# Performance work log

Measured on AMD Instinct MI355X. Metric: run time of the kernel, lower is better.

The kernel has to match this reference:

```python
import jax, jax.numpy as jnp
import numpy as np

C = 64
CR = C // 16  # reduction=16 -> query/key channels
B, H, W = 2, 80, 80


def setup_inputs() -> dict:
    key = jax.random.key(0)
    ks = jax.random.split(key, 13)
    s = 0.05
    return {
        "a": jax.random.normal(ks[0], (B, C, H, W), jnp.float32),
        "b": jax.random.normal(ks[1], (B, C, H, W), jnp.float32),
        "c": jax.random.normal(ks[2], (B, C, H, W), jnp.float32),
        # attentionAB (queries from a, keys from b)
        "wq_ab": jax.random.normal(ks[3], (CR, C), jnp.float32) * s,
        "bq_ab": jax.random.normal(ks[4], (CR,), jnp.float32) * s,
        "wk_ab": jax.random.normal(ks[5], (CR, C), jnp.float32) * s,
        "bk_ab": jax.random.normal(ks[6], (CR,), jnp.float32) * s,
        # attentionBC (queries from c, keys from b)
        "wq_bc": jax.random.normal(ks[7], (CR, C), jnp.float32) * s,
        "bq_bc": jax.random.normal(ks[8], (CR,), jnp.float32) * s,
        "wk_bc": jax.random.normal(ks[9], (CR, C), jnp.float32) * s,
        "bk_bc": jax.random.normal(ks[10], (CR,), jnp.float32) * s,
        # outer value conv on b
        "wv": jax.random.normal(ks[11], (C, C), jnp.float32) * s,
        "bv": jax.random.normal(ks[12], (C,), jnp.float32) * s,
    }


def _proj(x_flat, w, bias):
    # conv1x1 on flattened [B, C, N] -> [B, D, N]
    return jnp.einsum("dc,bcn->bdn", w, x_flat) + bias[None, :, None]


def _attention(x1_flat, x2_flat, wq, bq, wk, bk):
    q = _proj(x1_flat, wq, bq)  # [B, CR, N1]
    k = _proj(x2_flat, wk, bk)  # [B, CR, N2]
    scores = jnp.einsum("bdn,bdm->bnm", q, k)  # [B, N1, N2]
    return jax.nn.softmax(scores, axis=-1)


def reference(a, b, c, wq_ab, bq_ab, wk_ab, bk_ab, wq_bc, bq_bc, wk_bc, bk_bc, wv, bv):
    bsz, ch, h, w = b.shape
    n = h * w
    af = a.reshape(bsz, ch, n)
    bf = b.reshape(bsz, ch, n)
    cf = c.reshape(bsz, ch, n)

    attn_ba = _attention(af, bf, wq_ab, bq_ab, wk_ab, bk_ab)  # [B, Na, Nb]
    attn_bc = _attention(cf, bf, wq_bc, bq_bc, wk_bc, bk_bc)  # [B, Nc, Nb]

    values_b = _proj(bf, wv, bv)  # [B, C, Nb]

    # bmm(values_b, attn^T): contract over key positions m (of b)
    enh_ba = jnp.einsum("bcm,bnm->bcn", values_b, attn_ba)
    enh_bc = jnp.einsum("bcm,bnm->bcn", values_b, attn_bc)
    enhanced = (enh_ba + enh_bc) * 0.5
    return enhanced.reshape(bsz, ch, h, w)
```

## Files before the change

### kernel.cpp

```cpp
#include <hip/hip_runtime.h>
#include <hip/hip_bf16.h>

#define NPIX 6400
#define LOG2E 1.44269504088896340736f

typedef _Float16 half_t;
typedef _Float16 half4 __attribute__((ext_vector_type(4)));
typedef float float4x __attribute__((ext_vector_type(4)));


__global__ __launch_bounds__(256) void qk_proj_kernel(
    const float* __restrict__ a, const float* __restrict__ b, const float* __restrict__ c,
    const float* __restrict__ wq_ab, const float* __restrict__ bq_ab,
    const float* __restrict__ wk_ab, const float* __restrict__ bk_ab,
    const float* __restrict__ wq_bc, const float* __restrict__ bq_bc,
    const float* __restrict__ wk_bc, const float* __restrict__ bk_bc,
    half_t* __restrict__ qp, half_t* __restrict__ kp)
{
    int tid = blockIdx.x * 256 + threadIdx.x;
    int bz = tid / NPIX, n = tid % NPIX;
    const float* A = a + bz * 64 * NPIX + n;
    const float* B = b + bz * 64 * NPIX + n;
    const float* C = c + bz * 64 * NPIX + n;
    float qab[4] = {0,0,0,0}, kab[4] = {0,0,0,0}, qbc[4] = {0,0,0,0}, kbc[4] = {0,0,0,0};
    for (int ch = 0; ch < 64; ++ch) {
        float av = A[ch * NPIX], bv = B[ch * NPIX], cv = C[ch * NPIX];
#pragma unroll
        for (int d = 0; d < 4; ++d) {
            qab[d] += wq_ab[d * 64 + ch] * av;
            kab[d] += wk_ab[d * 64 + ch] * bv;
            qbc[d] += wq_bc[d * 64 + ch] * cv;
            kbc[d] += wk_bc[d * 64 + ch] * bv;
        }
    }
    half_t* q0 = qp + ((bz * 2 + 0) * NPIX + n) * 4;
    half_t* q1 = qp + ((bz * 2 + 1) * NPIX + n) * 4;
    half_t* k0 = kp + ((bz * 2 + 0) * NPIX + n) * 4;
    half_t* k1 = kp + ((bz * 2 + 1) * NPIX + n) * 4;
#pragma unroll
    for (int d = 0; d < 4; ++d) {
        q0[d] = (half_t)((qab[d] + bq_ab[d]) * LOG2E);
        q1[d] = (half_t)((qbc[d] + bq_bc[d]) * LOG2E);
        k0[d] = (half_t)(kab[d] + bk_ab[d]);
        k1[d] = (half_t)(kbc[d] + bk_bc[d]);
    }
}

__global__ __launch_bounds__(256) void v_proj_kernel(
    const float* __restrict__ b, const float* __restrict__ wv,
    const float* __restrict__ bvb, half_t* __restrict__ vp)
{
    int tid = blockIdx.x * 256 + threadIdx.x;
    int bz = tid / (64 * NPIX);
    int c  = (tid / NPIX) & 63;
    int n  = tid % NPIX;
    const float* B = b + bz * 64 * NPIX + n;
    float acc = bvb[c];
    for (int ch = 0; ch < 64; ++ch) acc += wv[c * 64 + ch] * B[ch * NPIX];
    vp[tid] = (half_t)acc;
}


__global__ __launch_bounds__(256) void attn_kernel(
    const half_t* __restrict__ qp, const half_t* __restrict__ kp,
    const half_t* __restrict__ vp, float* __restrict__ num, float* __restrict__ lsum)
{
    int idx = blockIdx.x;
    int qc = idx % 100;
    int br = (idx / 100) & 1;
    int bz = (idx / 200) & 1;
    int kh = idx / 400;
    int tid = threadIdx.x;
    int lane = tid & 63, w = tid >> 6;
    int g = lane >> 4, qi = lane & 15;
    int qbase = qc * 64 + w * 16;

    const half_t* Q = qp + ((bz * 2 + br) * NPIX + qbase) * 4;
    const half_t* K = kp + (bz * 2 + br) * NPIX * 4;
    const half_t* V = vp + bz * 64 * NPIX;

    half4 qf = {(half_t)0, (half_t)0, (half_t)0, (half_t)0};
    if (lane < 16) qf = *(const half4*)(Q + lane * 4);

    float4x accs[4] = {{0,0,0,0},{0,0,0,0},{0,0,0,0},{0,0,0,0}};
    float lrun = 0.f;

    __shared__ char lds[64 * 144];

    for (int chn = 0; chn < 50; ++chn) {
        int m0 = (kh * 50 + chn) * 64;
        __syncthreads();
#pragma unroll
        for (int si = 0; si < 2; ++si) {
            int s = tid + si * 256;
            int cc = s >> 3, so = s & 7;
            float4x seg = *(const float4x*)(V + cc * NPIX + m0 + so * 8);
            *(float4x*)(lds + cc * 144 + so * 16) = seg;
        }
        __syncthreads();
#pragma unroll
        for (int t = 0; t < 4; ++t) {
            int mt = m0 + t * 16;
            half4 kf = {(half_t)0, (half_t)0, (half_t)0, (half_t)0};
            if (lane < 16) kf = *(const half4*)(K + (mt + lane) * 4);
            float4x zero = {0.f, 0.f, 0.f, 0.f};
            float4x sc = __builtin_amdgcn_mfma_f32_16x16x16f16(kf, qf, zero, 0, 0, 0);
            float p0 = exp2f(sc[0]), p1 = exp2f(sc[1]), p2 = exp2f(sc[2]), p3 = exp2f(sc[3]);
            lrun += (p0 + p1) + (p2 + p3);
            half4 pf = {(half_t)p0, (half_t)p1, (half_t)p2, (half_t)p3};
            const char* lrow = lds + t * 32 + g * 8;
#pragma unroll
            for (int cb = 0; cb < 4; ++cb) {
                half4 vf = *(const half4*)(lrow + (cb * 16 + qi) * 144);
                accs[cb] = __builtin_amdgcn_mfma_f32_16x16x16f16(vf, pf, accs[cb], 0, 0, 0);
            }
        }
    }

    lrun += __shfl_xor(lrun, 16, 64);
    lrun += __shfl_xor(lrun, 32, 64);
    int q = qbase + qi;
    if (g == 0) atomicAdd(&lsum[(bz * 2 + br) * NPIX + q], lrun);

    float* numb = num + (bz * 2 + br) * 64 * NPIX;
#pragma unroll
    for (int cb = 0; cb < 4; ++cb)
#pragma unroll
        for (int r = 0; r < 4; ++r)
            atomicAdd(&numb[(cb * 16 + 4 * g + r) * NPIX + q], accs[cb][r]);
}

__global__ __launch_bounds__(256) void norm_kernel(
    const float* __restrict__ num, const float* __restrict__ lsum, float* __restrict__ out)
{
    int tid = blockIdx.x * 256 + threadIdx.x;
    int bz = tid / (64 * NPIX);
    int c  = (tid / NPIX) & 63;
    int n  = tid % NPIX;
    float lA = lsum[(bz * 2 + 0) * NPIX + n];
    float lC = lsum[(bz * 2 + 1) * NPIX + n];
    float vA = num[((bz * 2 + 0) * 64 + c) * NPIX + n];
    float vC = num[((bz * 2 + 1) * 64 + c) * NPIX + n];
    out[tid] = 0.5f * (vA / lA + vC / lC);
}

extern "C" void kernel_launch(void* const* d_in, const int* in_sizes, int n_in,
                              void* d_out, int out_size, void* d_ws, size_t ws_size,
                              hipStream_t stream) {
    (void)in_sizes; (void)n_in; (void)out_size; (void)ws_size;
    const float* a     = (const float*)d_in[0];
    const float* b     = (const float*)d_in[1];
    const float* c     = (const float*)d_in[2];
    const float* wq_ab = (const float*)d_in[3];
    const float* bq_ab = (const float*)d_in[4];
    const float* wk_ab = (const float*)d_in[5];
    const float* bk_ab = (const float*)d_in[6];
    const float* wq_bc = (const float*)d_in[7];
    const float* bq_bc = (const float*)d_in[8];
    const float* wk_bc = (const float*)d_in[9];
    const float* bk_bc = (const float*)d_in[10];
    const float* wv    = (const float*)d_in[11];
    const float* bv    = (const float*)d_in[12];
    float* out = (float*)d_out;

    half_t* qp = (half_t*)d_ws;
    half_t* kp = qp + 2 * 2 * NPIX * 4;
    half_t* vp = kp + 2 * 2 * NPIX * 4;
    float* num  = (float*)(vp + 2 * 64 * NPIX);
    float* lsum = num + 2 * 2 * 64 * NPIX;

    hipMemsetAsync(num, 0, (size_t)(2 * 2 * 64 * NPIX + 2 * 2 * NPIX) * sizeof(float), stream);

    qk_proj_kernel<<<50, 256, 0, stream>>>(a, b, c, wq_ab, bq_ab, wk_ab, bk_ab,
                                           wq_bc, bq_bc, wk_bc, bk_bc, qp, kp);
    v_proj_kernel<<<3200, 256, 0, stream>>>(b, wv, bv, vp);
    attn_kernel<<<800, 256, 0, stream>>>(qp, kp, vp, num, lsum);
    norm_kernel<<<3200, 256, 0, stream>>>(num, lsum, out);
}
```

Baseline: 220.3 us.

## Restructure attention with double-buffered LDS, two query tiles per wave, and vectorized projections

The attention kernel now handles 32 queries per wave across two MFMA tiles. This reuses each LDS V fragment and K fragment twice, and it splits keys into 4 chunks instead of 2. V tiles and K fragments are prefetched into registers and double-buffered in LDS so that one barrier per chunk overlaps loads with compute, and block indices are swizzled. The QK projection spreads the 4 output dims across threads for more parallelism, and the V projection and normalization are vectorized to float4 using a fast reciprocal. This raises register pressure and doubles the atomic contention on the numerator.

Result: faster. 213.4 us (-3.1%).

```diff
diff --git a/kernel.cpp b/kernel.cpp
--- a/kernel.cpp
+++ b/kernel.cpp
@@ -3,6 +3,10 @@
 
 #define NPIX 6400
 #define LOG2E 1.44269504088896340736f
+#define KH 4
+#define KEYS 1600
+#define NCH 25
+#define QF 2
 
 typedef _Float16 half_t;
 typedef _Float16 half4 __attribute__((ext_vector_type(4)));
@@ -18,32 +22,25 @@
     half_t* __restrict__ qp, half_t* __restrict__ kp)
 {
     int tid = blockIdx.x * 256 + threadIdx.x;
-    int bz = tid / NPIX, n = tid % NPIX;
+    int d = tid & 3;
+    int n = (tid >> 2) % NPIX;
+    int bz = (tid >> 2) / NPIX;
     const float* A = a + bz * 64 * NPIX + n;
     const float* B = b + bz * 64 * NPIX + n;
     const float* C = c + bz * 64 * NPIX + n;
-    float qab[4] = {0,0,0,0}, kab[4] = {0,0,0,0}, qbc[4] = {0,0,0,0}, kbc[4] = {0,0,0,0};
+    float qab = 0.f, kab = 0.f, qbc = 0.f, kbc = 0.f;
+#pragma unroll 4
     for (int ch = 0; ch < 64; ++ch) {
         float av = A[ch * NPIX], bv = B[ch * NPIX], cv = C[ch * NPIX];
-#pragma unroll
-        for (int d = 0; d < 4; ++d) {
-            qab[d] += wq_ab[d * 64 + ch] * av;
-            kab[d] += wk_ab[d * 64 + ch] * bv;
-            qbc[d] += wq_bc[d * 64 + ch] * cv;
-            kbc[d] += wk_bc[d * 64 + ch] * bv;
-        }
-    }
-    half_t* q0 = qp + ((bz * 2 + 0) * NPIX + n) * 4;
-    half_t* q1 = qp + ((bz * 2 + 1) * NPIX + n) * 4;
-    half_t* k0 = kp + ((bz * 2 + 0) * NPIX + n) * 4;
-    half_t* k1 = kp + ((bz * 2 + 1) * NPIX + n) * 4;
-#pragma unroll
-    for (int d = 0; d < 4; ++d) {
-        q0[d] = (half_t)((qab[d] + bq_ab[d]) * LOG2E);
-        q1[d] = (half_t)((qbc[d] + bq_bc[d]) * LOG2E);
-        k0[d] = (half_t)(kab[d] + bk_ab[d]);
-        k1[d] = (half_t)(kbc[d] + bk_bc[d]);
-    }
+        qab += wq_ab[d * 64 + ch] * av;
+        kab += wk_ab[d * 64 + ch] * bv;
+        qbc += wq_bc[d * 64 + ch] * cv;
+        kbc += wk_bc[d * 64 + ch] * bv;
+    }
+    qp[((bz * 2 + 0) * NPIX + n) * 4 + d] = (half_t)((qab + bq_ab[d]) * LOG2E);
+    qp[((bz * 2 + 1) * NPIX + n) * 4 + d] = (half_t)((qbc + bq_bc[d]) * LOG2E);
+    kp[((bz * 2 + 0) * NPIX + n) * 4 + d] = (half_t)(kab + bk_ab[d]);
+    kp[((bz * 2 + 1) * NPIX + n) * 4 + d] = (half_t)(kbc + bk_bc[d]);
 }
 
 __global__ __launch_bounds__(256) void v_proj_kernel(
@@ -51,13 +48,19 @@
     const float* __restrict__ bvb, half_t* __restrict__ vp)
 {
     int tid = blockIdx.x * 256 + threadIdx.x;
-    int bz = tid / (64 * NPIX);
-    int c  = (tid / NPIX) & 63;
-    int n  = tid % NPIX;
-    const float* B = b + bz * 64 * NPIX + n;
-    float acc = bvb[c];
-    for (int ch = 0; ch < 64; ++ch) acc += wv[c * 64 + ch] * B[ch * NPIX];
-    vp[tid] = (half_t)acc;
+    int n4 = tid % 1600;
+    int c  = (tid / 1600) & 63;
+    int bz = tid / (1600 * 64);
+    const float* B = b + bz * 64 * NPIX + n4 * 4;
+    float bias = bvb[c];
+    float4x acc = {bias, bias, bias, bias};
+    for (int ch = 0; ch < 64; ++ch) {
+        float4x bv = *(const float4x*)(B + ch * NPIX);
+        float wcc = wv[c * 64 + ch];
+        acc += wcc * bv;
+    }
+    half4 hv = {(half_t)acc[0], (half_t)acc[1], (half_t)acc[2], (half_t)acc[3]};
+    *(half4*)(vp + (bz * 64 + c) * NPIX + n4 * 4) = hv;
 }
 
 
@@ -65,83 +68,121 @@
     const half_t* __restrict__ qp, const half_t* __restrict__ kp,
     const half_t* __restrict__ vp, float* __restrict__ num, float* __restrict__ lsum)
 {
-    int idx = blockIdx.x;
-    int qc = idx % 100;
-    int br = (idx / 100) & 1;
-    int bz = (idx / 200) & 1;
-    int kh = idx / 400;
+    int bid = blockIdx.x;
+    int swz = (bid & 7) * 100 + (bid >> 3);
+    int qc = swz % 50;
+    int br = (swz / 50) & 1;
+    int bz = (swz / 100) & 1;
+    int kh = swz / 200;
+
     int tid = threadIdx.x;
     int lane = tid & 63, w = tid >> 6;
     int g = lane >> 4, qi = lane & 15;
-    int qbase = qc * 64 + w * 16;
+    int qbase = qc * 128 + w * 32;
 
     const half_t* Q = qp + ((bz * 2 + br) * NPIX + qbase) * 4;
-    const half_t* K = kp + (bz * 2 + br) * NPIX * 4;
-    const half_t* V = vp + bz * 64 * NPIX;
-
-    half4 qf = {(half_t)0, (half_t)0, (half_t)0, (half_t)0};
-    if (lane < 16) qf = *(const half4*)(Q + lane * 4);
-
-    float4x accs[4] = {{0,0,0,0},{0,0,0,0},{0,0,0,0},{0,0,0,0}};
-    float lrun = 0.f;
-
-    __shared__ char lds[64 * 144];
-
-    for (int chn = 0; chn < 50; ++chn) {
-        int m0 = (kh * 50 + chn) * 64;
-        __syncthreads();
-#pragma unroll
-        for (int si = 0; si < 2; ++si) {
-            int s = tid + si * 256;
-            int cc = s >> 3, so = s & 7;
-            float4x seg = *(const float4x*)(V + cc * NPIX + m0 + so * 8);
-            *(float4x*)(lds + cc * 144 + so * 16) = seg;
+    const half_t* K = kp + ((bz * 2 + br) * NPIX + kh * KEYS) * 4;
+    const half_t* V = vp + bz * 64 * NPIX + kh * KEYS;
+
+    half4 hz = {(half_t)0, (half_t)0, (half_t)0, (half_t)0};
+    half4 qf[QF];
+#pragma unroll
+    for (int i = 0; i < QF; ++i)
+        qf[i] = (lane < 16) ? *(const half4*)(Q + (i * 16 + lane) * 4) : hz;
+
+    float4x accs[QF][4] = {{{0,0,0,0},{0,0,0,0},{0,0,0,0},{0,0,0,0}},
+                           {{0,0,0,0},{0,0,0,0},{0,0,0,0},{0,0,0,0}}};
+    float lrun[QF] = {0.f, 0.f};
+
+    __shared__ char lds[2][64 * 144];
+    int cc0 = tid >> 3, so0 = tid & 7;
+    int cc1 = cc0 + 32;
+
+    float4x ga = *(const float4x*)(V + cc0 * NPIX + so0 * 8);
+    float4x gb = *(const float4x*)(V + cc1 * NPIX + so0 * 8);
+    half4 kc[4];
+#pragma unroll
+    for (int t = 0; t < 4; ++t)
+        kc[t] = (lane < 16) ? *(const half4*)(K + (t * 16 + lane) * 4) : hz;
+    *(float4x*)(lds[0] + cc0 * 144 + so0 * 16) = ga;
+    *(float4x*)(lds[0] + cc1 * 144 + so0 * 16) = gb;
+    __syncthreads();
+
+    int cur = 0;
+    for (int chn = 0; chn < NCH; ++chn) {
+        bool more = (chn + 1 < NCH);
+        float4x gna, gnb;
+        half4 kn[4];
+        if (more) {
+            int m0n = (chn + 1) * 64;
+            gna = *(const float4x*)(V + cc0 * NPIX + m0n + so0 * 8);
+            gnb = *(const float4x*)(V + cc1 * NPIX + m0n + so0 * 8);
+#pragma unroll
+            for (int t = 0; t < 4; ++t)
+                kn[t] = (lane < 16) ? *(const half4*)(K + (m0n + t * 16 + lane) * 4) : hz;
+        }
+        const char* lb = lds[cur];
+#pragma unroll
+        for (int t = 0; t < 4; ++t) {
+            half4 vf[4];
+#pragma unroll
+            for (int cb = 0; cb < 4; ++cb)
+                vf[cb] = *(const half4*)(lb + (cb * 16 + qi) * 144 + t * 32 + g * 8);
+#pragma unroll
+            for (int i = 0; i < QF; ++i) {
+                float4x zero = {0.f, 0.f, 0.f, 0.f};
+                float4x sc = __builtin_amdgcn_mfma_f32_16x16x16f16(kc[t], qf[i], zero, 0, 0, 0);
+                float p0 = exp2f(sc[0]), p1 = exp2f(sc[1]), p2 = exp2f(sc[2]), p3 = exp2f(sc[3]);
+                lrun[i] += (p0 + p1) + (p2 + p3);
+                half4 pf = {(half_t)p0, (half_t)p1, (half_t)p2, (half_t)p3};
+#pragma unroll
+                for (int cb = 0; cb < 4; ++cb)
+                    accs[i][cb] = __builtin_amdgcn_mfma_f32_16x16x16f16(vf[cb], pf, accs[i][cb], 0, 0, 0);
+            }
+        }
+        if (more) {
+            *(float4x*)(lds[cur ^ 1] + cc0 * 144 + so0 * 16) = gna;
+            *(float4x*)(lds[cur ^ 1] + cc1 * 144 + so0 * 16) = gnb;
+#pragma unroll
+            for (int t = 0; t < 4; ++t) kc[t] = kn[t];
         }
         __syncthreads();
-#pragma unroll
-        for (int t = 0; t < 4; ++t) {
-            int mt = m0 + t * 16;
-            half4 kf = {(half_t)0, (half_t)0, (half_t)0, (half_t)0};
-            if (lane < 16) kf = *(const half4*)(K + (mt + lane) * 4);
-            float4x zero = {0.f, 0.f, 0.f, 0.f};
-            float4x sc = __builtin_amdgcn_mfma_f32_16x16x16f16(kf, qf, zero, 0, 0, 0);
-            float p0 = exp2f(sc[0]), p1 = exp2f(sc[1]), p2 = exp2f(sc[2]), p3 = exp2f(sc[3]);
-            lrun += (p0 + p1) + (p2 + p3);
-            half4 pf = {(half_t)p0, (half_t)p1, (half_t)p2, (half_t)p3};
-            const char* lrow = lds + t * 32 + g * 8;
-#pragma unroll
-            for (int cb = 0; cb < 4; ++cb) {
-                half4 vf = *(const half4*)(lrow + (cb * 16 + qi) * 144);
-                accs[cb] = __builtin_amdgcn_mfma_f32_16x16x16f16(vf, pf, accs[cb], 0, 0, 0);
-            }
-        }
-    }
-
-    lrun += __shfl_xor(lrun, 16, 64);
-    lrun += __shfl_xor(lrun, 32, 64);
-    int q = qbase + qi;
-    if (g == 0) atomicAdd(&lsum[(bz * 2 + br) * NPIX + q], lrun);
+        cur ^= 1;
+    }
 
     float* numb = num + (bz * 2 + br) * 64 * NPIX;
 #pragma unroll
-    for (int cb = 0; cb < 4; ++cb)
-#pragma unroll
-        for (int r = 0; r < 4; ++r)
-            atomicAdd(&numb[(cb * 16 + 4 * g + r) * NPIX + q], accs[cb][r]);
+    for (int i = 0; i < QF; ++i) {
+        float l = lrun[i];
+        l += __shfl_xor(l, 16, 64);
+        l += __shfl_xor(l, 32, 64);
+        int q = qbase + i * 16 + qi;
+        if (g == 0) atomicAdd(&lsum[(bz * 2 + br) * NPIX + q], l);
+#pragma unroll
+        for (int cb = 0; cb < 4; ++cb)
+#pragma unroll
+            for (int r = 0; r < 4; ++r)
+                atomicAdd(&numb[(cb * 16 + 4 * g + r) * NPIX + q], accs[i][cb][r]);
+    }
 }
 
 __global__ __launch_bounds__(256) void norm_kernel(
     const float* __restrict__ num, const float* __restrict__ lsum, float* __restrict__ out)
 {
     int tid = blockIdx.x * 256 + threadIdx.x;
-    int bz = tid / (64 * NPIX);
-    int c  = (tid / NPIX) & 63;
-    int n  = tid % NPIX;
-    float lA = lsum[(bz * 2 + 0) * NPIX + n];
-    float lC = lsum[(bz * 2 + 1) * NPIX + n];
-    float vA = num[((bz * 2 + 0) * 64 + c) * NPIX + n];
-    float vC = num[((bz * 2 + 1) * 64 + c) * NPIX + n];
-    out[tid] = 0.5f * (vA / lA + vC / lC);
+    int n4 = tid % 1600;
+    int c  = (tid / 1600) & 63;
+    int bz = tid / (1600 * 64);
+    float4x lA = *(const float4x*)(lsum + (bz * 2 + 0) * NPIX + n4 * 4);
+    float4x lC = *(const float4x*)(lsum + (bz * 2 + 1) * NPIX + n4 * 4);
+    float4x vA = *(const float4x*)(num + ((bz * 2 + 0) * 64 + c) * NPIX + n4 * 4);
+    float4x vC = *(const float4x*)(num + ((bz * 2 + 1) * 64 + c) * NPIX + n4 * 4);
+    float4x r;
+#pragma unroll
+    for (int j = 0; j < 4; ++j)
+        r[j] = 0.5f * (vA[j] * __builtin_amdgcn_rcpf(lA[j]) +
+                       vC[j] * __builtin_amdgcn_rcpf(lC[j]));
+    *(float4x*)(out + (bz * 64 + c) * NPIX + n4 * 4) = r;
 }
 
 extern "C" void kernel_launch(void* const* d_in, const int* in_sizes, int n_in,
@@ -171,9 +212,9 @@
 
     hipMemsetAsync(num, 0, (size_t)(2 * 2 * 64 * NPIX + 2 * 2 * NPIX) * sizeof(float), stream);
 
-    qk_proj_kernel<<<50, 256, 0, stream>>>(a, b, c, wq_ab, bq_ab, wk_ab, bk_ab,
-                                           wq_bc, bq_bc, wk_bc, bk_bc, qp, kp);
-    v_proj_kernel<<<3200, 256, 0, stream>>>(b, wv, bv, vp);
+    qk_proj_kernel<<<200, 256, 0, stream>>>(a, b, c, wq_ab, bq_ab, wk_ab, bk_ab,
+                                            wq_bc, bq_bc, wk_bc, bk_bc, qp, kp);
+    v_proj_kernel<<<800, 256, 0, stream>>>(b, wv, bv, vp);
     attn_kernel<<<800, 256, 0, stream>>>(qp, kp, vp, num, lsum);
-    norm_kernel<<<3200, 256, 0, stream>>>(num, lsum, out);
-}
+    norm_kernel<<<800, 256, 0, stream>>>(num, lsum, out);
+}
```
